# Optimization experiments

Hardware: AMD Instinct MI355X
Metric: run time of the kernel (lower is better)

## Reference

```python
import jax, jax.numpy as jnp
import numpy as np

B, T, F1, F2 = 16384, 5, 300, 251
IN, H = 551, 128

def setup_inputs() -> dict:
    key = jax.random.key(0)
    ks = jax.random.split(key, 16)
    s = 0.05
    return {
        "x1": jax.random.normal(ks[0], (B, T, F1), jnp.float32),
        "x2": jax.random.normal(ks[1], (B, T, F2), jnp.float32),
        "W_ih": jax.random.normal(ks[2], (4 * H, IN), jnp.float32) * s,
        "W_hh": jax.random.normal(ks[3], (4 * H, H), jnp.float32) * s,
        "b_ih": jax.random.normal(ks[4], (4 * H,), jnp.float32) * s,
        "b_hh": jax.random.normal(ks[5], (4 * H,), jnp.float32) * s,
        "W1": jax.random.normal(ks[6], (531, H * T), jnp.float32) * s,
        "b1": jax.random.normal(ks[7], (531,), jnp.float32) * s,
        "W2": jax.random.normal(ks[8], (256, 531), jnp.float32) * s,
        "b2": jax.random.normal(ks[9], (256,), jnp.float32) * s,
        "W3": jax.random.normal(ks[10], (64, 256), jnp.float32) * s,
        "b3": jax.random.normal(ks[11], (64,), jnp.float32) * s,
        "W4": jax.random.normal(ks[12], (2, 64), jnp.float32) * s,
        "b4": jax.random.normal(ks[13], (2,), jnp.float32) * s,
    }

def _lstm(x, W_ih, W_hh, b_ih, b_hh):
    # x: [B, T, IN] -> outputs [B, T, H]; PyTorch gate order i, f, g, o
    xg = jnp.einsum('bti,gi->btg', x, W_ih) + b_ih + b_hh  # [B, T, 4H]
    xg = jnp.transpose(xg, (1, 0, 2))  # [T, B, 4H]
    h0 = jnp.zeros((x.shape[0], H), x.dtype)
    c0 = jnp.zeros((x.shape[0], H), x.dtype)

    def step(carry, xg_t):
        h, c = carry
        g = xg_t + h @ W_hh.T  # [B, 4H]
        i, f, gg, o = jnp.split(g, 4, axis=-1)
        c = jax.nn.sigmoid(f) * c + jax.nn.sigmoid(i) * jnp.tanh(gg)
        h = jax.nn.sigmoid(o) * jnp.tanh(c)
        return (h, c), h

    _, hs = jax.lax.scan(step, (h0, c0), xg)  # hs: [T, B, H]
    return jnp.transpose(hs, (1, 0, 2))

def reference(x1, x2, W_ih, W_hh, b_ih, b_hh, W1, b1, W2, b2, W3, b3, W4, b4):
    x = jnp.concatenate((x1, x2), axis=2)  # [B, T, 551]
    h = _lstm(x, W_ih, W_hh, b_ih, b_hh)   # [B, T, H]
    h = h.reshape(h.shape[0], T * H)
    h = jax.nn.relu(h @ W1.T + b1)
    h = jax.nn.relu(h @ W2.T + b2)
    h = jax.nn.relu(h @ W3.T + b3)
    logits = h @ W4.T + b4
    return jax.nn.softmax(logits, axis=1)
```

## Files before the change

### kernel.cpp

```cpp
#include <hip/hip_runtime.h>
#include <hip/hip_bf16.h>


typedef short  short8  __attribute__((ext_vector_type(8)));
typedef float  f32x4   __attribute__((ext_vector_type(4)));

#define MFMA(a, b, c) __builtin_amdgcn_mfma_f32_16x16x32_bf16((a), (b), (c), 0, 0, 0)

__device__ __forceinline__ short f2bs(float f) {
    __hip_bfloat16 h = __float2bfloat16(f);
    union { __hip_bfloat16 h; short s; } u; u.h = h; return u.s;
}
__device__ __forceinline__ float b2f(short s) {
    union { unsigned u; float f; } v; v.u = ((unsigned)(unsigned short)s) << 16; return v.f;
}
__device__ __forceinline__ float sigf(float x)  { return 1.f / (1.f + __expf(-x)); }
__device__ __forceinline__ float mytanh(float x){ return 2.f / (1.f + __expf(-2.f * x)) - 1.f; }

#define TT     5
#define F1     300
#define F2     251
#define INF    551
#define G4     512
#define HH     128
#define FLAT   640
#define L1N    531
#define L1KP   544
#define L2N    256

#define O_WIH  0u
#define O_WHH  589824u
#define O_W1   720896u
#define O_W2   1458176u
#define O_W3   1736704u
#define O_BG   1769472u
#define O_B1   1771520u
#define WS_NEED 1773824u

#define SM_TOTAL 39424
#define AFL_STR  648
#define A1_OFF   20736
#define A1_STR   584
#define A2_OFF   0
#define A2_STR   264
#define A3_OFF   8448
#define A3_STR   72

__device__ __forceinline__ void pack_b(const float* __restrict__ W, short* __restrict__ dst,
                                       int i, int tpn, int Nsrc, int Ksrc, int ldw)
{
    int tile = i >> 9, rem = i & 511, lane = rem >> 3, jj = rem & 7;
    int tn = tile / tpn, tk = tile - tn * tpn;
    int n = tn * 16 + (lane & 15);
    int k = tk * 32 + (lane >> 4) * 8 + jj;
    float v = (n < Nsrc && k < Ksrc) ? W[n * ldw + k] : 0.f;
    dst[i] = f2bs(v);
}

__global__ void prep_kernel(
    const float* __restrict__ W_ih, const float* __restrict__ W_hh,
    const float* __restrict__ b_ih, const float* __restrict__ b_hh,
    const float* __restrict__ W1,   const float* __restrict__ b1,
    const float* __restrict__ W2,   const float* __restrict__ W3,
    short* __restrict__ Wihp, short* __restrict__ Whhp, float* __restrict__ biasg,
    short* __restrict__ W1p,  float* __restrict__ b1p,  short* __restrict__ W2p,
    short* __restrict__ W3p)
{
    const int N0 = G4 * 576;
    const int N1 = N0 + G4 * HH;
    const int N2 = N1 + 576 * FLAT;
    const int N3 = N2 + L2N * L1KP;
    const int N4 = N3 + 64 * L2N;
    const int N5 = N4 + G4;
    const int N6 = N5 + 576;
    const int stride = gridDim.x * blockDim.x;
    for (int i = blockIdx.x * blockDim.x + threadIdx.x; i < N6; i += stride) {
        if (i < N0)      pack_b(W_ih, Wihp, i,       18, G4,  INF, INF);
        else if (i < N1) pack_b(W_hh, Whhp, i - N0,   4, G4,  HH,  HH);
        else if (i < N2) pack_b(W1,   W1p,  i - N1,  20, L1N, FLAT, FLAT);
        else if (i < N3) pack_b(W2,   W2p,  i - N2,  17, L2N, L1N, L1N);
        else if (i < N4) pack_b(W3,   W3p,  i - N3,   8, 64,  L2N, L2N);
        else if (i < N5) { int j = i - N4; biasg[j] = b_ih[j] + b_hh[j]; }
        else             { int j = i - N5; b1p[j] = (j < L1N) ? b1[j] : 0.f; }
    }
}

__global__ __launch_bounds__(512, 2) void fused_kernel(
    const float* __restrict__ x1, const float* __restrict__ x2,
    const short* __restrict__ Wihp, const short* __restrict__ Whhp,
    const float* __restrict__ biasg,
    const short* __restrict__ W1p, const float* __restrict__ b1p,
    const short* __restrict__ W2p, const float* __restrict__ b2,
    const short* __restrict__ W3p, const float* __restrict__ b3,
    const float* __restrict__ W4,  const float* __restrict__ b4,
    float* __restrict__ out)
{
    __shared__ __align__(16) short sA[SM_TOTAL];
    const int tid  = threadIdx.x;
    const int w    = tid >> 6;
    const int lane = tid & 63;
    const int quad = lane >> 4;
    const int c16  = lane & 15;
    const int b0   = blockIdx.x * 32;
    const int j    = w * 16 + c16;

    float bg[4];
#pragma unroll
    for (int g = 0; g < 4; ++g) bg[g] = biasg[g * HH + j];

    short8 whh[4][4];
#pragma unroll
    for (int g = 0; g < 4; ++g)
#pragma unroll
        for (int ks = 0; ks < 4; ++ks)
            whh[g][ks] = *(const short8*)&Whhp[((((g * 8 + w) * 4) + ks) << 9) + lane * 8];

    float cst[2][4];
#pragma unroll
    for (int mt = 0; mt < 2; ++mt)
#pragma unroll
        for (int r = 0; r < 4; ++r) cst[mt][r] = 0.f;

    for (int t = 0; t < TT; ++t) {
        const float* x1r[2];
        const float* x2r[2];
#pragma unroll
        for (int mt = 0; mt < 2; ++mt) {
            int brow = b0 + mt * 16 + c16;
            x1r[mt] = x1 + (brow * TT + t) * F1;
            x2r[mt] = x2 + (brow * TT + t) * F2;
        }

        f32x4 acc[2][4];
#pragma unroll
        for (int mt = 0; mt < 2; ++mt)
#pragma unroll
            for (int g = 0; g < 4; ++g)
                acc[mt][g] = (f32x4){0.f, 0.f, 0.f, 0.f};

        float4 cur0[2], cur1[2];
#pragma unroll
        for (int mt = 0; mt < 2; ++mt) {
            int k0 = quad * 8;
            cur0[mt] = (k0     < F1) ? *(const float4*)(x1r[mt] + k0)
                                     : *(const float4*)(x2r[mt] + (k0 - F1));
            cur1[mt] = (k0 + 4 < F1) ? *(const float4*)(x1r[mt] + k0 + 4)
                                     : *(const float4*)(x2r[mt] + (k0 + 4 - F1));
        }
        for (int tk = 0; tk < 17; ++tk) {
            short8 afr[2];
#pragma unroll
            for (int mt = 0; mt < 2; ++mt) {
                afr[mt][0] = f2bs(cur0[mt].x); afr[mt][1] = f2bs(cur0[mt].y);
                afr[mt][2] = f2bs(cur0[mt].z); afr[mt][3] = f2bs(cur0[mt].w);
                afr[mt][4] = f2bs(cur1[mt].x); afr[mt][5] = f2bs(cur1[mt].y);
                afr[mt][6] = f2bs(cur1[mt].z); afr[mt][7] = f2bs(cur1[mt].w);
            }
            if (tk < 16) {
#pragma unroll
                for (int mt = 0; mt < 2; ++mt) {
                    int k0 = (tk + 1) * 32 + quad * 8;
                    cur0[mt] = (k0     < F1) ? *(const float4*)(x1r[mt] + k0)
                                             : *(const float4*)(x2r[mt] + (k0 - F1));
                    cur1[mt] = (k0 + 4 < F1) ? *(const float4*)(x1r[mt] + k0 + 4)
                                             : *(const float4*)(x2r[mt] + (k0 + 4 - F1));
                }
            }
#pragma unroll
            for (int g = 0; g < 4; ++g) {
                short8 bfr = *(const short8*)&Wihp[(((g * 8 + w) * 18 + tk) << 9) + lane * 8];
                acc[0][g] = MFMA(afr[0], bfr, acc[0][g]);
                acc[1][g] = MFMA(afr[1], bfr, acc[1][g]);
            }
        }
        {
            short8 afr[2];
#pragma unroll
            for (int mt = 0; mt < 2; ++mt) {
#pragma unroll
                for (int jj = 0; jj < 8; ++jj) {
                    int k = 544 + quad * 8 + jj;
                    afr[mt][jj] = (k < INF) ? f2bs(x2r[mt][k - F1]) : (short)0;
                }
            }
#pragma unroll
            for (int g = 0; g < 4; ++g) {
                short8 bfr = *(const short8*)&Wihp[(((g * 8 + w) * 18 + 17) << 9) + lane * 8];
                acc[0][g] = MFMA(afr[0], bfr, acc[0][g]);
                acc[1][g] = MFMA(afr[1], bfr, acc[1][g]);
            }
        }

        if (t > 0) {
#pragma unroll
            for (int ks = 0; ks < 4; ++ks) {
                short8 ha[2];
#pragma unroll
                for (int mt = 0; mt < 2; ++mt)
                    ha[mt] = *(const short8*)
                        &sA[(mt * 16 + c16) * AFL_STR + (t - 1) * HH + ks * 32 + quad * 8];
#pragma unroll
                for (int g = 0; g < 4; ++g) {
                    acc[0][g] = MFMA(ha[0], whh[g][ks], acc[0][g]);
                    acc[1][g] = MFMA(ha[1], whh[g][ks], acc[1][g]);
                }
            }
        }

#pragma unroll
        for (int mt = 0; mt < 2; ++mt) {
#pragma unroll
            for (int r = 0; r < 4; ++r) {
                int m = mt * 16 + quad * 4 + r;
                float gi = acc[mt][0][r] + bg[0];
                float gf = acc[mt][1][r] + bg[1];
                float gg = acc[mt][2][r] + bg[2];
                float go = acc[mt][3][r] + bg[3];
                float cn = sigf(gf) * cst[mt][r] + sigf(gi) * mytanh(gg);
                cst[mt][r] = cn;
                sA[m * AFL_STR + t * HH + j] = f2bs(sigf(go) * mytanh(cn));
            }
        }
        __syncthreads();
    }

    {
        const int ntc = (w < 4) ? 5 : 4;
        f32x4 acc1[2][5];
#pragma unroll
        for (int mt = 0; mt < 2; ++mt)
#pragma unroll
            for (int i = 0; i < 5; ++i)
                acc1[mt][i] = (f32x4){0.f, 0.f, 0.f, 0.f};
        for (int ks = 0; ks < 20; ++ks) {
            short8 a[2];
#pragma unroll
            for (int mt = 0; mt < 2; ++mt)
                a[mt] = *(const short8*)&sA[(mt * 16 + c16) * AFL_STR + ks * 32 + quad * 8];
#pragma unroll
            for (int i = 0; i < 5; ++i) {
                if (i < ntc) {
                    int tn = w + 8 * i;
                    short8 b = *(const short8*)&W1p[((tn * 20 + ks) << 9) + lane * 8];
                    acc1[0][i] = MFMA(a[0], b, acc1[0][i]);
                    acc1[1][i] = MFMA(a[1], b, acc1[1][i]);
                }
            }
        }
        __syncthreads();
#pragma unroll
        for (int i = 0; i < 5; ++i) {
            if (i < ntc) {
                int tn = w + 8 * i;
                int n  = tn * 16 + c16;
                float bv = b1p[n];
#pragma unroll
                for (int mt = 0; mt < 2; ++mt)
#pragma unroll
                    for (int r = 0; r < 4; ++r) {
                        int m = mt * 16 + quad * 4 + r;
                        float v = acc1[mt][i][r] + bv;
                        sA[A1_OFF + m * A1_STR + n] = f2bs(v > 0.f ? v : 0.f);
                    }
            }
        }
    }
    __syncthreads();

    {
        f32x4 acc2[2][2];
#pragma unroll
        for (int mt = 0; mt < 2; ++mt)
#pragma unroll
            for (int i = 0; i < 2; ++i)
                acc2[mt][i] = (f32x4){0.f, 0.f, 0.f, 0.f};
        for (int ks = 0; ks < 17; ++ks) {
            short8 a[2];
#pragma unroll
            for (int mt = 0; mt < 2; ++mt)
                a[mt] = *(const short8*)&sA[A1_OFF + (mt * 16 + c16) * A1_STR + ks * 32 + quad * 8];
#pragma unroll
            for (int i = 0; i < 2; ++i) {
                int tn = w * 2 + i;
                short8 b = *(const short8*)&W2p[((tn * 17 + ks) << 9) + lane * 8];
                acc2[0][i] = MFMA(a[0], b, acc2[0][i]);
                acc2[1][i] = MFMA(a[1], b, acc2[1][i]);
            }
        }
#pragma unroll
        for (int i = 0; i < 2; ++i) {
            int n = (w * 2 + i) * 16 + c16;
            float bv = b2[n];
#pragma unroll
            for (int mt = 0; mt < 2; ++mt)
#pragma unroll
                for (int r = 0; r < 4; ++r) {
                    int m = mt * 16 + quad * 4 + r;
                    float v = acc2[mt][i][r] + bv;
                    sA[A2_OFF + m * A2_STR + n] = f2bs(v > 0.f ? v : 0.f);
                }
        }
    }
    __syncthreads();

    if (w < 4) {
        f32x4 acc3[2];
        acc3[0] = (f32x4){0.f, 0.f, 0.f, 0.f};
        acc3[1] = (f32x4){0.f, 0.f, 0.f, 0.f};
#pragma unroll
        for (int ks = 0; ks < 8; ++ks) {
            short8 a[2];
#pragma unroll
            for (int mt = 0; mt < 2; ++mt)
                a[mt] = *(const short8*)&sA[A2_OFF + (mt * 16 + c16) * A2_STR + ks * 32 + quad * 8];
            short8 b = *(const short8*)&W3p[((w * 8 + ks) << 9) + lane * 8];
            acc3[0] = MFMA(a[0], b, acc3[0]);
            acc3[1] = MFMA(a[1], b, acc3[1]);
        }
        int n = w * 16 + c16;
        float bv = b3[n];
#pragma unroll
        for (int mt = 0; mt < 2; ++mt)
#pragma unroll
            for (int r = 0; r < 4; ++r) {
                int m = mt * 16 + quad * 4 + r;
                float v = acc3[mt][r] + bv;
                sA[A3_OFF + m * A3_STR + n] = f2bs(v > 0.f ? v : 0.f);
            }
    }
    __syncthreads();

    if (tid < 64) {
        int m   = tid >> 1;
        int cls = tid & 1;
        float s = b4[cls];
#pragma unroll 8
        for (int k = 0; k < 64; ++k)
            s += b2f(sA[A3_OFF + m * A3_STR + k]) * W4[cls * 64 + k];
        float other = __shfl_xor(s, 1);
        float p = 1.f / (1.f + __expf(other - s));
        out[(b0 + m) * 2 + cls] = p;
    }
}

extern "C" void kernel_launch(void* const* d_in, const int* in_sizes, int n_in,
                              void* d_out, int out_size, void* d_ws, size_t ws_size,
                              hipStream_t stream)
{
    (void)in_sizes; (void)n_in; (void)out_size;
    if (ws_size < (size_t)WS_NEED) return;

    const float* x1   = (const float*)d_in[0];
    const float* x2   = (const float*)d_in[1];
    const float* W_ih = (const float*)d_in[2];
    const float* W_hh = (const float*)d_in[3];
    const float* b_ih = (const float*)d_in[4];
    const float* b_hh = (const float*)d_in[5];
    const float* W1   = (const float*)d_in[6];
    const float* b1   = (const float*)d_in[7];
    const float* W2   = (const float*)d_in[8];
    const float* b2   = (const float*)d_in[9];
    const float* W3   = (const float*)d_in[10];
    const float* b3   = (const float*)d_in[11];
    const float* W4   = (const float*)d_in[12];
    const float* b4   = (const float*)d_in[13];

    char* ws = (char*)d_ws;
    short* Wihp  = (short*)(ws + O_WIH);
    short* Whhp  = (short*)(ws + O_WHH);
    short* W1p   = (short*)(ws + O_W1);
    short* W2p   = (short*)(ws + O_W2);
    short* W3p   = (short*)(ws + O_W3);
    float* biasg = (float*)(ws + O_BG);
    float* b1p   = (float*)(ws + O_B1);

    prep_kernel<<<3461, 256, 0, stream>>>(W_ih, W_hh, b_ih, b_hh, W1, b1, W2, W3,
                                          Wihp, Whhp, biasg, W1p, b1p, W2p, W3p);
    fused_kernel<<<512, 512, 0, stream>>>(x1, x2, Wihp, Whhp, biasg,
                                          W1p, b1p, W2p, b2, W3p, b3, W4, b4,
                                          (float*)d_out);
}
```

Baseline: 442.9 us.

## Pre-pack activations to bf16 MFMA fragments in a staging kernel

```diff
diff --git a/kernel.cpp b/kernel.cpp
--- a/kernel.cpp
+++ b/kernel.cpp
@@ -3,6 +3,7 @@
 
 
 typedef short  short8  __attribute__((ext_vector_type(8)));
+typedef short  short4v __attribute__((ext_vector_type(4)));
 typedef float  f32x4   __attribute__((ext_vector_type(4)));
 
 #define MFMA(a, b, c) __builtin_amdgcn_mfma_f32_16x16x32_bf16((a), (b), (c), 0, 0, 0)
@@ -28,6 +29,9 @@
 #define L1KP   544
 #define L2N    256
 
+#define NXPACK 512
+#define NPREP  448
+
 #define O_WIH  0u
 #define O_WHH  589824u
 #define O_W1   720896u
@@ -35,7 +39,8 @@
 #define O_W3   1736704u
 #define O_BG   1769472u
 #define O_B1   1771520u
-#define WS_NEED 1773824u
+#define O_XP   1773824u
+#define WS_NEED 96145664u
 
 #define SM_TOTAL 39424
 #define AFL_STR  648
@@ -57,36 +62,83 @@
     dst[i] = f2bs(v);
 }
 
-__global__ void prep_kernel(
+__global__ __launch_bounds__(256, 4) void stage_kernel(
+    const float* __restrict__ x1, const float* __restrict__ x2,
     const float* __restrict__ W_ih, const float* __restrict__ W_hh,
     const float* __restrict__ b_ih, const float* __restrict__ b_hh,
     const float* __restrict__ W1,   const float* __restrict__ b1,
     const float* __restrict__ W2,   const float* __restrict__ W3,
     short* __restrict__ Wihp, short* __restrict__ Whhp, float* __restrict__ biasg,
     short* __restrict__ W1p,  float* __restrict__ b1p,  short* __restrict__ W2p,
-    short* __restrict__ W3p)
+    short* __restrict__ W3p,  short* __restrict__ xp)
 {
-    const int N0 = G4 * 576;
-    const int N1 = N0 + G4 * HH;
-    const int N2 = N1 + 576 * FLAT;
-    const int N3 = N2 + L2N * L1KP;
-    const int N4 = N3 + 64 * L2N;
-    const int N5 = N4 + G4;
-    const int N6 = N5 + 576;
-    const int stride = gridDim.x * blockDim.x;
-    for (int i = blockIdx.x * blockDim.x + threadIdx.x; i < N6; i += stride) {
-        if (i < N0)      pack_b(W_ih, Wihp, i,       18, G4,  INF, INF);
-        else if (i < N1) pack_b(W_hh, Whhp, i - N0,   4, G4,  HH,  HH);
-        else if (i < N2) pack_b(W1,   W1p,  i - N1,  20, L1N, FLAT, FLAT);
-        else if (i < N3) pack_b(W2,   W2p,  i - N2,  17, L2N, L1N, L1N);
-        else if (i < N4) pack_b(W3,   W3p,  i - N3,   8, 64,  L2N, L2N);
-        else if (i < N5) { int j = i - N4; biasg[j] = b_ih[j] + b_hh[j]; }
-        else             { int j = i - N5; b1p[j] = (j < L1N) ? b1[j] : 0.f; }
-    }
-}
-
-__global__ __launch_bounds__(512, 2) void fused_kernel(
-    const float* __restrict__ x1, const float* __restrict__ x2,
+    __shared__ __align__(16) short sX[32][584];
+    const int tid = threadIdx.x;
+
+    if (blockIdx.x < NXPACK) {
+        const int b0 = blockIdx.x * 32;
+        for (int idx = tid; idx < 32 * 32; idx += 256) {
+            int r = idx >> 5, c = 544 + (idx & 31);
+            sX[r][c] = 0;
+        }
+        __syncthreads();
+
+        const int r  = tid >> 3;
+        const int c8 = tid & 7;
+        const int lane = tid & 63;
+        const int wv   = tid >> 6;
+
+        for (int t = 0; t < TT; ++t) {
+            {
+                const float* xr = x1 + ((b0 + r) * TT + t) * F1;
+#pragma unroll 4
+                for (int c4 = c8; c4 < 75; c4 += 8) {
+                    float4 v = *(const float4*)(xr + c4 * 4);
+                    short4v s;
+                    s[0] = f2bs(v.x); s[1] = f2bs(v.y); s[2] = f2bs(v.z); s[3] = f2bs(v.w);
+                    *(short4v*)&sX[r][c4 * 4] = s;
+                }
+            }
+            {
+                const float* xr = x2 + ((b0 + r) * TT + t) * F2;
+#pragma unroll 8
+                for (int c = c8; c < F2; c += 8)
+                    sX[r][F1 + c] = f2bs(xr[c]);
+            }
+            __syncthreads();
+#pragma unroll
+            for (int i = 0; i < 9; ++i) {
+                int tau = wv + i * 4;
+                int tm  = (tau >= 18) ? 1 : 0;
+                int kt  = tau - tm * 18;
+                short8 v = *(const short8*)&sX[tm * 16 + (lane & 15)][kt * 32 + (lane >> 4) * 8];
+                *(short8*)&xp[(((blockIdx.x * 2 + tm) * TT + t) * 18 + kt) * 512 + lane * 8] = v;
+            }
+            __syncthreads();
+        }
+    } else {
+        const int N0 = G4 * 576;
+        const int N1 = N0 + G4 * HH;
+        const int N2 = N1 + 576 * FLAT;
+        const int N3 = N2 + L2N * L1KP;
+        const int N4 = N3 + 64 * L2N;
+        const int N5 = N4 + G4;
+        const int N6 = N5 + 576;
+        const int stride = NPREP * 256;
+        for (int i = (blockIdx.x - NXPACK) * 256 + tid; i < N6; i += stride) {
+            if (i < N0)      pack_b(W_ih, Wihp, i,       18, G4,  INF, INF);
+            else if (i < N1) pack_b(W_hh, Whhp, i - N0,   4, G4,  HH,  HH);
+            else if (i < N2) pack_b(W1,   W1p,  i - N1,  20, L1N, FLAT, FLAT);
+            else if (i < N3) pack_b(W2,   W2p,  i - N2,  17, L2N, L1N, L1N);
+            else if (i < N4) pack_b(W3,   W3p,  i - N3,   8, 64,  L2N, L2N);
+            else if (i < N5) { int j = i - N4; biasg[j] = b_ih[j] + b_hh[j]; }
+            else             { int j = i - N5; b1p[j] = (j < L1N) ? b1[j] : 0.f; }
+        }
+    }
+}
+
+__global__ __launch_bounds__(512, 4) void fused_kernel(
+    const short* __restrict__ xp,
     const short* __restrict__ Wihp, const short* __restrict__ Whhp,
     const float* __restrict__ biasg,
     const short* __restrict__ W1p, const float* __restrict__ b1p,
@@ -122,15 +174,6 @@
         for (int r = 0; r < 4; ++r) cst[mt][r] = 0.f;
 
     for (int t = 0; t < TT; ++t) {
-        const float* x1r[2];
-        const float* x2r[2];
-#pragma unroll
-        for (int mt = 0; mt < 2; ++mt) {
-            int brow = b0 + mt * 16 + c16;
-            x1r[mt] = x1 + (brow * TT + t) * F1;
-            x2r[mt] = x2 + (brow * TT + t) * F2;
-        }
-
         f32x4 acc[2][4];
 #pragma unroll
         for (int mt = 0; mt < 2; ++mt)
@@ -138,56 +181,25 @@
             for (int g = 0; g < 4; ++g)
                 acc[mt][g] = (f32x4){0.f, 0.f, 0.f, 0.f};
 
-        float4 cur0[2], cur1[2];
-#pragma unroll
-        for (int mt = 0; mt < 2; ++mt) {
-            int k0 = quad * 8;
-            cur0[mt] = (k0     < F1) ? *(const float4*)(x1r[mt] + k0)
-                                     : *(const float4*)(x2r[mt] + (k0 - F1));
-            cur1[mt] = (k0 + 4 < F1) ? *(const float4*)(x1r[mt] + k0 + 4)
-                                     : *(const float4*)(x2r[mt] + (k0 + 4 - F1));
-        }
-        for (int tk = 0; tk < 17; ++tk) {
-            short8 afr[2];
-#pragma unroll
-            for (int mt = 0; mt < 2; ++mt) {
-                afr[mt][0] = f2bs(cur0[mt].x); afr[mt][1] = f2bs(cur0[mt].y);
-                afr[mt][2] = f2bs(cur0[mt].z); afr[mt][3] = f2bs(cur0[mt].w);
-                afr[mt][4] = f2bs(cur1[mt].x); afr[mt][5] = f2bs(cur1[mt].y);
-                afr[mt][6] = f2bs(cur1[mt].z); afr[mt][7] = f2bs(cur1[mt].w);
-            }
-            if (tk < 16) {
-#pragma unroll
-                for (int mt = 0; mt < 2; ++mt) {
-                    int k0 = (tk + 1) * 32 + quad * 8;
-                    cur0[mt] = (k0     < F1) ? *(const float4*)(x1r[mt] + k0)
-                                             : *(const float4*)(x2r[mt] + (k0 - F1));
-                    cur1[mt] = (k0 + 4 < F1) ? *(const float4*)(x1r[mt] + k0 + 4)
-                                             : *(const float4*)(x2r[mt] + (k0 + 4 - F1));
-                }
-            }
-#pragma unroll
-            for (int g = 0; g < 4; ++g) {
-                short8 bfr = *(const short8*)&Wihp[(((g * 8 + w) * 18 + tk) << 9) + lane * 8];
-                acc[0][g] = MFMA(afr[0], bfr, acc[0][g]);
-                acc[1][g] = MFMA(afr[1], bfr, acc[1][g]);
-            }
-        }
         {
-            short8 afr[2];
-#pragma unroll
-            for (int mt = 0; mt < 2; ++mt) {
-#pragma unroll
-                for (int jj = 0; jj < 8; ++jj) {
-                    int k = 544 + quad * 8 + jj;
-                    afr[mt][jj] = (k < INF) ? f2bs(x2r[mt][k - F1]) : (short)0;
-                }
-            }
-#pragma unroll
-            for (int g = 0; g < 4; ++g) {
-                short8 bfr = *(const short8*)&Wihp[(((g * 8 + w) * 18 + 17) << 9) + lane * 8];
-                acc[0][g] = MFMA(afr[0], bfr, acc[0][g]);
-                acc[1][g] = MFMA(afr[1], bfr, acc[1][g]);
+            const short* xpt0 = xp + ((blockIdx.x * 2 + 0) * TT + t) * 18 * 512 + lane * 8;
+            const short* xpt1 = xp + ((blockIdx.x * 2 + 1) * TT + t) * 18 * 512 + lane * 8;
+            short8 a0 = *(const short8*)(xpt0);
+            short8 a1 = *(const short8*)(xpt1);
+#pragma unroll
+            for (int tk = 0; tk < 18; ++tk) {
+                short8 na0, na1;
+                if (tk < 17) {
+                    na0 = *(const short8*)(xpt0 + (tk + 1) * 512);
+                    na1 = *(const short8*)(xpt1 + (tk + 1) * 512);
+                }
+#pragma unroll
+                for (int g = 0; g < 4; ++g) {
+                    short8 bfr = *(const short8*)&Wihp[(((g * 8 + w) * 18 + tk) << 9) + lane * 8];
+                    acc[0][g] = MFMA(a0, bfr, acc[0][g]);
+                    acc[1][g] = MFMA(a1, bfr, acc[1][g]);
+                }
+                a0 = na0; a1 = na1;
             }
         }
 
@@ -373,10 +385,12 @@
     short* W3p   = (short*)(ws + O_W3);
     float* biasg = (float*)(ws + O_BG);
     float* b1p   = (float*)(ws + O_B1);
-
-    prep_kernel<<<3461, 256, 0, stream>>>(W_ih, W_hh, b_ih, b_hh, W1, b1, W2, W3,
-                                          Wihp, Whhp, biasg, W1p, b1p, W2p, W3p);
-    fused_kernel<<<512, 512, 0, stream>>>(x1, x2, Wihp, Whhp, biasg,
-                                          W1p, b1p, W2p, b2, W3p, b3, W4, b4,
-                                          (float*)d_out);
-}
+    short* xp    = (short*)(ws + O_XP);
+
+    stage_kernel<<<NXPACK + NPREP, 256, 0, stream>>>(
+        x1, x2, W_ih, W_hh, b_ih, b_hh, W1, b1, W2, W3,
+        Wihp, Whhp, biasg, W1p, b1p, W2p, W3p, xp);
+    fused_kernel<<<512, 512, 0, stream>>>(
+        xp, Wihp, Whhp, biasg, W1p, b1p, W2p, b2, W3p, b3, W4, b4,
+        (float*)d_out);
+}
```

New measurement: 723.6 us. 1.63x slower.
